# Kernel tuning notes

Hardware: AMD Instinct MI355X
Metric: run time of the kernel (lower is better)

The kernel has to match this reference:

```python
import jax, jax.numpy as jnp
import numpy as np

N_EMBD = 1024
HEAD_SIZE = 128

def setup_inputs() -> dict:
    key = jax.random.key(0)
    k1, k2, k3, k4 = jax.random.split(key, 4)
    x = jax.random.normal(k1, (8, 2048, N_EMBD), dtype=jnp.float32)
    # Linear(n_embd, head_size, bias=False): y = x @ W, W: [n_embd, head_size]
    s = 1.0 / np.sqrt(N_EMBD)
    Wk = jax.random.uniform(k2, (N_EMBD, HEAD_SIZE), jnp.float32, -s, s)
    Wq = jax.random.uniform(k3, (N_EMBD, HEAD_SIZE), jnp.float32, -s, s)
    Wv = jax.random.uniform(k4, (N_EMBD, HEAD_SIZE), jnp.float32, -s, s)
    return {"x": x, "Wk": Wk, "Wq": Wq, "Wv": Wv}

def reference(x, Wk, Wq, Wv):
    B, T, C = x.shape
    H = Wk.shape[1]
    k = jnp.einsum('btc,ch->bth', x, Wk)
    q = jnp.einsum('btc,ch->bth', x, Wq)
    v = jnp.einsum('btc,ch->bth', x, Wv)
    # scores [B, T, T], causal mask, scaled by head_size**-0.5
    wei = jnp.einsum('bqh,bkh->bqk', q, k) * (H ** -0.5)
    causal = jnp.tril(jnp.ones((T, T), dtype=bool))
    wei = jnp.where(causal, wei, -jnp.inf)
    wei = jax.nn.softmax(wei, axis=-1)
    # dropout p=0.0 (eval mode): identity
    out = jnp.einsum('bqk,bkh->bqh', wei, v)
    return out
```

## Files before the change

### kernel.cpp

```cpp
#include <hip/hip_runtime.h>
#include <hip/hip_bf16.h>
#include <stdint.h>

typedef short v8s __attribute__((ext_vector_type(8)));
typedef float v4f __attribute__((ext_vector_type(4)));
typedef float v16f __attribute__((ext_vector_type(16)));

#define N_EMBD 1024
#define HEAD 128
#define TOKENS 16384
#define T_SEQ 2048
#define BATCH 8
#define BPB 96

__device__ __forceinline__ short f2bf(float f) {
    union { float f; uint32_t u; } c; c.f = f;
    uint32_t u = c.u;
    uint32_t r = (u + 0x7fffu + ((u >> 16) & 1u)) >> 16;
    return (short)r;
}

__device__ __forceinline__ float bf2f(short s) {
    union { uint32_t u; float f; } c; c.u = ((uint32_t)(uint16_t)s) << 16;
    return c.f;
}

__global__ __launch_bounds__(256)
void wt_kernel(const float* __restrict__ Wq, const float* __restrict__ Wk,
               const float* __restrict__ Wv, short* __restrict__ wt) {
    int tid = blockIdx.x * 256 + threadIdx.x;
    int w   = tid >> 17;
    int rem = tid & 131071;
    int c = rem >> 7, h = rem & 127;
    const float* src = (w == 0) ? Wq : ((w == 1) ? Wk : Wv);
    wt[w * 131072 + h * 1024 + c] = f2bf(src[rem]);
}

__global__ __launch_bounds__(256)
void qkv_gemm(const float* __restrict__ x, const short* __restrict__ wt,
              short* __restrict__ qkv, short* __restrict__ vT) {
    const int bid = blockIdx.x;
    const int xcd = bid & 7, q = bid >> 3;
    const int mt  = xcd * 32 + q / 3;
    const int w   = q % 3;
    const int m0  = mt * 64;

    __shared__ short smem[2][64 * 40 + 128 * 40];

    const int t = threadIdx.x;
    const int lane = t & 63, wv = t >> 6;
    const int l31 = lane & 31, l1 = lane >> 5;
    const int wm = wv & 1, wn = wv >> 1;

    const short* wtw = wt + w * 131072;

    const int arow = t >> 3, ac4 = t & 7;
    const int brow = t >> 2, bc8 = t & 3;
    const float* aptr0 = x + (size_t)(m0 + arow) * 1024 + ac4 * 4;
    const float* aptr1 = x + (size_t)(m0 + arow + 32) * 1024 + ac4 * 4;
    const short* bptr0 = wtw + brow * 1024 + bc8 * 8;
    const short* bptr1 = wtw + (brow + 64) * 1024 + bc8 * 8;

    float4 af0 = *(const float4*)aptr0;
    float4 af1 = *(const float4*)aptr1;
    uint4  bf0 = *(const uint4*)bptr0;
    uint4  bf1 = *(const uint4*)bptr1;

    v16f acc[2];
    for (int i = 0; i < 16; ++i) { acc[0][i] = 0.f; acc[1][i] = 0.f; }

    {
        short* sA = smem[0]; short* sB = smem[0] + 64 * 40;
        union { short s[4]; uint64_t u; } p0, p1;
        p0.s[0] = f2bf(af0.x); p0.s[1] = f2bf(af0.y); p0.s[2] = f2bf(af0.z); p0.s[3] = f2bf(af0.w);
        p1.s[0] = f2bf(af1.x); p1.s[1] = f2bf(af1.y); p1.s[2] = f2bf(af1.z); p1.s[3] = f2bf(af1.w);
        *(uint64_t*)(&sA[arow * 40 + ac4 * 4]) = p0.u;
        *(uint64_t*)(&sA[(arow + 32) * 40 + ac4 * 4]) = p1.u;
        *(uint4*)(&sB[brow * 40 + bc8 * 8]) = bf0;
        *(uint4*)(&sB[(brow + 64) * 40 + bc8 * 8]) = bf1;
    }

    for (int it = 0; it < 32; ++it) {
        if (it < 31) {
            int kk = (it + 1) * 32;
            af0 = *(const float4*)(aptr0 + kk);
            af1 = *(const float4*)(aptr1 + kk);
            bf0 = *(const uint4*)(bptr0 + kk);
            bf1 = *(const uint4*)(bptr1 + kk);
        }
        __syncthreads();
        const short* sA = smem[it & 1];
        const short* sB = smem[it & 1] + 64 * 40;
        for (int ks = 0; ks < 2; ++ks) {
            v8s a = *(const v8s*)&sA[(wm * 32 + l31) * 40 + ks * 16 + l1 * 8];
            for (int ni = 0; ni < 2; ++ni) {
                v8s b = *(const v8s*)&sB[(wn * 64 + ni * 32 + l31) * 40 + ks * 16 + l1 * 8];
                acc[ni] = __builtin_amdgcn_mfma_f32_32x32x16_bf16(a, b, acc[ni], 0, 0, 0);
            }
        }
        if (it < 31) {
            short* nA = smem[(it + 1) & 1];
            short* nB = smem[(it + 1) & 1] + 64 * 40;
            union { short s[4]; uint64_t u; } p0, p1;
            p0.s[0] = f2bf(af0.x); p0.s[1] = f2bf(af0.y); p0.s[2] = f2bf(af0.z); p0.s[3] = f2bf(af0.w);
            p1.s[0] = f2bf(af1.x); p1.s[1] = f2bf(af1.y); p1.s[2] = f2bf(af1.z); p1.s[3] = f2bf(af1.w);
            *(uint64_t*)(&nA[arow * 40 + ac4 * 4]) = p0.u;
            *(uint64_t*)(&nA[(arow + 32) * 40 + ac4 * 4]) = p1.u;
            *(uint4*)(&nB[brow * 40 + bc8 * 8]) = bf0;
            *(uint4*)(&nB[(brow + 64) * 40 + bc8 * 8]) = bf1;
        }
    }

    if (w < 2) {
        short* outw = qkv + (size_t)w * TOKENS * HEAD;
        for (int ni = 0; ni < 2; ++ni) {
            int col = wn * 64 + ni * 32 + l31;
            for (int reg = 0; reg < 16; ++reg) {
                int m = (reg & 3) + 8 * (reg >> 2) + 4 * l1;
                outw[(size_t)(m0 + wm * 32 + m) * HEAD + col] = f2bf(acc[ni][reg]);
            }
        }
    } else {
        __syncthreads();
        short* sT = (short*)smem;
        for (int ni = 0; ni < 2; ++ni) {
            int col = wn * 64 + ni * 32 + l31;
            for (int g = 0; g < 4; ++g) {
                union { short s[4]; uint64_t u; } pk;
                for (int r = 0; r < 4; ++r) pk.s[r] = f2bf(acc[ni][g * 4 + r]);
                *(uint64_t*)(&sT[col * 72 + wm * 32 + 8 * g + 4 * l1]) = pk.u;
            }
        }
        __syncthreads();
        for (int it = 0; it < 4; ++it) {
            int c = it * 256 + t;
            int col = c >> 3, c8 = c & 7;
            uint4 d = *(const uint4*)(&sT[col * 72 + c8 * 8]);
            *(uint4*)(&vT[(size_t)col * TOKENS + m0 + c8 * 8]) = d;
        }
    }
}

__global__ __launch_bounds__(256)
void attn_kernel(const short* __restrict__ qb, const short* __restrict__ kb,
                 const short* __restrict__ vT, short* __restrict__ po,
                 float* __restrict__ pl) {
    const int bid = blockIdx.x;
    const int b  = bid & 7;
    const int r0 = bid >> 3;
    int qt2 = 0, c0 = 0;
    for (;;) { int sz = (2 * qt2 + 4) / 3; if (r0 < c0 + sz) break; c0 += sz; ++qt2; }
    const int s = r0 - c0;
    const int q0 = qt2 * 128;
    const int nkt = 2 * qt2 + 2;
    const int kt0 = s * 3;
    const int kt1 = (kt0 + 3 < nkt) ? (kt0 + 3) : nkt;

    __shared__ short sK[64 * 128];
    __shared__ short sV[128 * 64];
    __shared__ short sP[128 * 72];

    const int t = threadIdx.x;
    const int wv = t >> 6, lane = t & 63, ln = lane & 15, qd = lane >> 4;
    const int wrow0 = q0 + wv * 32;

    v8s qf[2][4];
    for (int qg = 0; qg < 2; ++qg) {
        const short* qrow = qb + ((size_t)(b * T_SEQ + wrow0 + qg * 16 + ln)) * HEAD;
        for (int ks = 0; ks < 4; ++ks)
            qf[qg][ks] = *(const v8s*)(qrow + ks * 32 + qd * 8);
    }

    v4f o[2][8] = {};
    float rs[2] = {0.f, 0.f};
    const float sc = 1.4426950408889634f / 11.313708498984761f;

    for (int kt = kt0; kt < kt1; ++kt) {
        __syncthreads();
        const short* kbase = kb + ((size_t)(b * T_SEQ + kt * 64)) * HEAD;
        for (int it = 0; it < 4; ++it) {
            int c = it * 256 + t;
            int row = c >> 4, ch = c & 15;
            uint4 d = *(const uint4*)(kbase + row * HEAD + ch * 8);
            int sch = (ch & 8) | ((ch ^ row) & 7);
            *(uint4*)(&sK[row * 128 + sch * 8]) = d;
        }
        const short* vbase = vT + (size_t)(b * T_SEQ + kt * 64);
        for (int it = 0; it < 4; ++it) {
            int c = it * 256 + t;
            int dd = c >> 3, ch = c & 7;
            uint4 d = *(const uint4*)(vbase + (size_t)dd * TOKENS + ch * 8);
            *(uint4*)(&sV[dd * 64 + ((ch ^ dd) & 7) * 8]) = d;
        }
        __syncthreads();

        if (kt * 64 >= wrow0 + 32) continue;

        v4f st[2][4] = {};
        for (int ni = 0; ni < 4; ++ni) {
            int krow = ni * 16 + ln;
            for (int ks = 0; ks < 4; ++ks) {
                int ch = ks * 4 + qd;
                v8s kf = *(const v8s*)&sK[krow * 128 + ((ch & 8) | ((ch ^ krow) & 7)) * 8];
                st[0][ni] = __builtin_amdgcn_mfma_f32_16x16x32_bf16(kf, qf[0][ks], st[0][ni], 0, 0, 0);
                st[1][ni] = __builtin_amdgcn_mfma_f32_16x16x32_bf16(kf, qf[1][ks], st[1][ni], 0, 0, 0);
            }
        }

        const bool needMask = (kt * 64 + 63 > wrow0);
        for (int qg = 0; qg < 2; ++qg) {
            int prow = wv * 32 + qg * 16 + ln;
            int qrow_g = wrow0 + qg * 16 + ln;
            for (int ni = 0; ni < 4; ++ni) {
                union { short s[4]; uint64_t u; } pk;
                for (int r = 0; r < 4; ++r) {
                    float p = exp2f(st[qg][ni][r] * sc);
                    int kg = kt * 64 + ni * 16 + qd * 4 + r;
                    if (needMask && kg > qrow_g) p = 0.f;
                    rs[qg] += p;
                    pk.s[r] = f2bf(p);
                }
                *(uint64_t*)(&sP[prow * 72 + ni * 16 + qd * 4]) = pk.u;
            }
        }

        for (int kk2 = 0; kk2 < 2; ++kk2) {
            v8s pf0 = *(const v8s*)&sP[(wv * 32 + ln) * 72 + kk2 * 32 + qd * 8];
            v8s pf1 = *(const v8s*)&sP[(wv * 32 + 16 + ln) * 72 + kk2 * 32 + qd * 8];
            for (int oni = 0; oni < 8; ++oni) {
                int dd = oni * 16 + ln;
                int ch = kk2 * 4 + qd;
                v8s vf = *(const v8s*)&sV[dd * 64 + ((ch ^ dd) & 7) * 8];
                o[0][oni] = __builtin_amdgcn_mfma_f32_16x16x32_bf16(vf, pf0, o[0][oni], 0, 0, 0);
                o[1][oni] = __builtin_amdgcn_mfma_f32_16x16x32_bf16(vf, pf1, o[1][oni], 0, 0, 0);
            }
        }
    }

    float lsum[2];
    for (int qg = 0; qg < 2; ++qg) {
        float v = rs[qg];
        v += __shfl_xor(v, 16);
        v += __shfl_xor(v, 32);
        lsum[qg] = v;
    }

    short* pob = po + (size_t)bid * 128 * 128;
    for (int qg = 0; qg < 2; ++qg)
        for (int oni = 0; oni < 8; ++oni) {
            union { short s[4]; uint2 u; } pk;
            for (int r = 0; r < 4; ++r) pk.s[r] = f2bf(o[qg][oni][r]);
            *(uint2*)(&pob[(((qg * 8 + oni) * 4 + wv) * 64 + lane) * 4]) = pk.u;
        }
    if (lane < 16)
        for (int qg = 0; qg < 2; ++qg)
            pl[bid * 128 + wv * 32 + qg * 16 + lane] = lsum[qg];
}

__global__ __launch_bounds__(256)
void combine_kernel(const short* __restrict__ po, const float* __restrict__ pl,
                    float* __restrict__ out) {
    const int bid = blockIdx.x;
    const int dh  = bid & 1;
    const int qh  = (bid >> 1) & 1;
    const int qt2 = (bid >> 2) & 15;
    const int b   = bid >> 6;
    int cum = 0;
    for (int j = 0; j < qt2; ++j) cum += (2 * j + 4) / 3;
    const int S = (2 * qt2 + 4) / 3;

    const int t = threadIdx.x;
    const int wv = t >> 6, lane = t & 63, ln = lane & 15, qd = lane >> 4;

    float l = 0.f;
    float accv[4][4] = {};

    for (int si = 0; si < S; ++si) {
        int slot = (cum + si) * 8 + b;
        l += pl[slot * 128 + wv * 32 + qh * 16 + ln];
        const short* pob = po + (size_t)slot * 16384;
        for (int oi = 0; oi < 4; ++oi) {
            int oni = dh * 4 + oi;
            union { short s[4]; uint2 u; } pk;
            pk.u = *(const uint2*)(&pob[(((qh * 8 + oni) * 4 + wv) * 64 + lane) * 4]);
            for (int r = 0; r < 4; ++r) accv[oi][r] += bf2f(pk.s[r]);
        }
    }
    float inv = 1.f / l;
    float* ob = out + ((size_t)(b * T_SEQ) + qt2 * 128 + wv * 32 + qh * 16 + ln) * HEAD;
    for (int oi = 0; oi < 4; ++oi) {
        float4 o4 = make_float4(accv[oi][0] * inv, accv[oi][1] * inv,
                                accv[oi][2] * inv, accv[oi][3] * inv);
        *(float4*)(ob + (dh * 4 + oi) * 16 + qd * 4) = o4;
    }
}

extern "C" void kernel_launch(void* const* d_in, const int* in_sizes, int n_in,
                              void* d_out, int out_size, void* d_ws, size_t ws_size,
                              hipStream_t stream) {
    const float* x  = (const float*)d_in[0];
    const float* Wk = (const float*)d_in[1];
    const float* Wq = (const float*)d_in[2];
    const float* Wv = (const float*)d_in[3];
    float* out = (float*)d_out;

    char* ws = (char*)d_ws;
    short* wt = (short*)ws;
    short* qb = (short*)(ws + 0x100000u);
    short* kb = (short*)(ws + 0x500000u);
    short* vT = (short*)(ws + 0x900000u);
    short* po = (short*)(ws + 0xD00000u);
    float* pl = (float*)(ws + 0x2500000u);
    short* qkv = qb;

    wt_kernel<<<1536, 256, 0, stream>>>(Wq, Wk, Wv, wt);
    qkv_gemm<<<768, 256, 0, stream>>>(x, wt, qkv, vT);
    attn_kernel<<<BATCH * BPB, 256, 0, stream>>>(qb, kb, vT, po, pl);
    combine_kernel<<<512, 256, 0, stream>>>(po, pl, out);
}
```

Before: 168.8 us.

## Enlarge QKV GEMM tiles and prefetch K/V tiles into registers in attention

The QKV projection GEMM moves from 64x128 tiles with a K-step of 32 to 128x128 tiles with a K-step of 64. Each wave now computes a 2x2 grid of 32x32 MFMA accumulators and the grid shrinks to 384 blocks, which improves operand reuse and halves the number of barriers. The attention kernel now loads the next K/V tile into registers after the barrier so the global loads overlap the current tile's compute, instead of loading and then storing directly. In exchange, register use rises (launch_bounds 256,2), the GEMM needs more shared memory, and fewer blocks run in the GEMM.

```diff
diff --git a/kernel.cpp b/kernel.cpp
--- a/kernel.cpp
+++ b/kernel.cpp
@@ -36,106 +36,110 @@
     wt[w * 131072 + h * 1024 + c] = f2bf(src[rem]);
 }
 
-__global__ __launch_bounds__(256)
+__global__ __launch_bounds__(256, 2)
 void qkv_gemm(const float* __restrict__ x, const short* __restrict__ wt,
               short* __restrict__ qkv, short* __restrict__ vT) {
     const int bid = blockIdx.x;
     const int xcd = bid & 7, q = bid >> 3;
-    const int mt  = xcd * 32 + q / 3;
-    const int w   = q % 3;
-    const int m0  = mt * 64;
-
-    __shared__ short smem[2][64 * 40 + 128 * 40];
+    const int mtl = q / 3, w = q % 3;
+    const int mt  = xcd * 16 + mtl;
+    const int m0  = mt * 128;
+
+    __shared__ short smem[2][256 * 72];
 
     const int t = threadIdx.x;
-    const int lane = t & 63, wv = t >> 6;
+    const int wv = t >> 6, lane = t & 63;
     const int l31 = lane & 31, l1 = lane >> 5;
     const int wm = wv & 1, wn = wv >> 1;
 
     const short* wtw = wt + w * 131072;
 
-    const int arow = t >> 3, ac4 = t & 7;
-    const int brow = t >> 2, bc8 = t & 3;
-    const float* aptr0 = x + (size_t)(m0 + arow) * 1024 + ac4 * 4;
-    const float* aptr1 = x + (size_t)(m0 + arow + 32) * 1024 + ac4 * 4;
-    const short* bptr0 = wtw + brow * 1024 + bc8 * 8;
-    const short* bptr1 = wtw + (brow + 64) * 1024 + bc8 * 8;
-
-    float4 af0 = *(const float4*)aptr0;
-    float4 af1 = *(const float4*)aptr1;
-    uint4  bf0 = *(const uint4*)bptr0;
-    uint4  bf1 = *(const uint4*)bptr1;
-
-    v16f acc[2];
-    for (int i = 0; i < 16; ++i) { acc[0][i] = 0.f; acc[1][i] = 0.f; }
+    const int ar = t >> 4, ac = t & 15;
+    const int br = t >> 3, bc = t & 7;
+    const float* aptr = x + (size_t)(m0 + ar) * 1024 + ac * 4;
+    const short* bptr = wtw + br * 1024 + bc * 8;
+
+    float4 af[8]; uint4 bfr[4];
+    for (int i = 0; i < 8; ++i) af[i] = *(const float4*)(aptr + (size_t)i * 16 * 1024);
+    for (int i = 0; i < 4; ++i) bfr[i] = *(const uint4*)(bptr + (size_t)i * 32 * 1024);
+
+    v16f acc[2][2];
+    for (int i = 0; i < 16; ++i) {
+        acc[0][0][i] = 0.f; acc[0][1][i] = 0.f; acc[1][0][i] = 0.f; acc[1][1][i] = 0.f;
+    }
 
     {
-        short* sA = smem[0]; short* sB = smem[0] + 64 * 40;
-        union { short s[4]; uint64_t u; } p0, p1;
-        p0.s[0] = f2bf(af0.x); p0.s[1] = f2bf(af0.y); p0.s[2] = f2bf(af0.z); p0.s[3] = f2bf(af0.w);
-        p1.s[0] = f2bf(af1.x); p1.s[1] = f2bf(af1.y); p1.s[2] = f2bf(af1.z); p1.s[3] = f2bf(af1.w);
-        *(uint64_t*)(&sA[arow * 40 + ac4 * 4]) = p0.u;
-        *(uint64_t*)(&sA[(arow + 32) * 40 + ac4 * 4]) = p1.u;
-        *(uint4*)(&sB[brow * 40 + bc8 * 8]) = bf0;
-        *(uint4*)(&sB[(brow + 64) * 40 + bc8 * 8]) = bf1;
-    }
-
-    for (int it = 0; it < 32; ++it) {
-        if (it < 31) {
-            int kk = (it + 1) * 32;
-            af0 = *(const float4*)(aptr0 + kk);
-            af1 = *(const float4*)(aptr1 + kk);
-            bf0 = *(const uint4*)(bptr0 + kk);
-            bf1 = *(const uint4*)(bptr1 + kk);
+        short* sA = smem[0]; short* sB = smem[0] + 128 * 72;
+        for (int i = 0; i < 8; ++i) {
+            union { short s[4]; uint64_t u; } p;
+            p.s[0] = f2bf(af[i].x); p.s[1] = f2bf(af[i].y);
+            p.s[2] = f2bf(af[i].z); p.s[3] = f2bf(af[i].w);
+            *(uint64_t*)&sA[(i * 16 + ar) * 72 + ac * 4] = p.u;
+        }
+        for (int i = 0; i < 4; ++i)
+            *(uint4*)&sB[(i * 32 + br) * 72 + bc * 8] = bfr[i];
+    }
+
+    for (int it = 0; it < 16; ++it) {
+        if (it < 15) {
+            int kk = (it + 1) * 64;
+            for (int i = 0; i < 8; ++i) af[i] = *(const float4*)(aptr + (size_t)i * 16 * 1024 + kk);
+            for (int i = 0; i < 4; ++i) bfr[i] = *(const uint4*)(bptr + (size_t)i * 32 * 1024 + kk);
         }
         __syncthreads();
         const short* sA = smem[it & 1];
-        const short* sB = smem[it & 1] + 64 * 40;
-        for (int ks = 0; ks < 2; ++ks) {
-            v8s a = *(const v8s*)&sA[(wm * 32 + l31) * 40 + ks * 16 + l1 * 8];
-            for (int ni = 0; ni < 2; ++ni) {
-                v8s b = *(const v8s*)&sB[(wn * 64 + ni * 32 + l31) * 40 + ks * 16 + l1 * 8];
-                acc[ni] = __builtin_amdgcn_mfma_f32_32x32x16_bf16(a, b, acc[ni], 0, 0, 0);
-            }
-        }
-        if (it < 31) {
+        const short* sB = smem[it & 1] + 128 * 72;
+        for (int ks = 0; ks < 4; ++ks) {
+            v8s a0 = *(const v8s*)&sA[(wm * 64 + l31) * 72 + ks * 16 + l1 * 8];
+            v8s a1 = *(const v8s*)&sA[(wm * 64 + 32 + l31) * 72 + ks * 16 + l1 * 8];
+            v8s b0 = *(const v8s*)&sB[(wn * 64 + l31) * 72 + ks * 16 + l1 * 8];
+            v8s b1 = *(const v8s*)&sB[(wn * 64 + 32 + l31) * 72 + ks * 16 + l1 * 8];
+            acc[0][0] = __builtin_amdgcn_mfma_f32_32x32x16_bf16(a0, b0, acc[0][0], 0, 0, 0);
+            acc[0][1] = __builtin_amdgcn_mfma_f32_32x32x16_bf16(a0, b1, acc[0][1], 0, 0, 0);
+            acc[1][0] = __builtin_amdgcn_mfma_f32_32x32x16_bf16(a1, b0, acc[1][0], 0, 0, 0);
+            acc[1][1] = __builtin_amdgcn_mfma_f32_32x32x16_bf16(a1, b1, acc[1][1], 0, 0, 0);
+        }
+        if (it < 15) {
             short* nA = smem[(it + 1) & 1];
-            short* nB = smem[(it + 1) & 1] + 64 * 40;
-            union { short s[4]; uint64_t u; } p0, p1;
-            p0.s[0] = f2bf(af0.x); p0.s[1] = f2bf(af0.y); p0.s[2] = f2bf(af0.z); p0.s[3] = f2bf(af0.w);
-            p1.s[0] = f2bf(af1.x); p1.s[1] = f2bf(af1.y); p1.s[2] = f2bf(af1.z); p1.s[3] = f2bf(af1.w);
-            *(uint64_t*)(&nA[arow * 40 + ac4 * 4]) = p0.u;
-            *(uint64_t*)(&nA[(arow + 32) * 40 + ac4 * 4]) = p1.u;
-            *(uint4*)(&nB[brow * 40 + bc8 * 8]) = bf0;
-            *(uint4*)(&nB[(brow + 64) * 40 + bc8 * 8]) = bf1;
+            short* nB = smem[(it + 1) & 1] + 128 * 72;
+            for (int i = 0; i < 8; ++i) {
+                union { short s[4]; uint64_t u; } p;
+                p.s[0] = f2bf(af[i].x); p.s[1] = f2bf(af[i].y);
+                p.s[2] = f2bf(af[i].z); p.s[3] = f2bf(af[i].w);
+                *(uint64_t*)&nA[(i * 16 + ar) * 72 + ac * 4] = p.u;
+            }
+            for (int i = 0; i < 4; ++i)
+                *(uint4*)&nB[(i * 32 + br) * 72 + bc * 8] = bfr[i];
         }
     }
 
     if (w < 2) {
         short* outw = qkv + (size_t)w * TOKENS * HEAD;
-        for (int ni = 0; ni < 2; ++ni) {
-            int col = wn * 64 + ni * 32 + l31;
-            for (int reg = 0; reg < 16; ++reg) {
-                int m = (reg & 3) + 8 * (reg >> 2) + 4 * l1;
-                outw[(size_t)(m0 + wm * 32 + m) * HEAD + col] = f2bf(acc[ni][reg]);
-            }
-        }
+        for (int mi = 0; mi < 2; ++mi)
+            for (int ni = 0; ni < 2; ++ni) {
+                int col = wn * 64 + ni * 32 + l31;
+                for (int reg = 0; reg < 16; ++reg) {
+                    int m = (reg & 3) + 8 * (reg >> 2) + 4 * l1;
+                    outw[(size_t)(m0 + wm * 64 + mi * 32 + m) * HEAD + col] = f2bf(acc[mi][ni][reg]);
+                }
+            }
     } else {
         __syncthreads();
         short* sT = (short*)smem;
-        for (int ni = 0; ni < 2; ++ni) {
-            int col = wn * 64 + ni * 32 + l31;
-            for (int g = 0; g < 4; ++g) {
-                union { short s[4]; uint64_t u; } pk;
-                for (int r = 0; r < 4; ++r) pk.s[r] = f2bf(acc[ni][g * 4 + r]);
-                *(uint64_t*)(&sT[col * 72 + wm * 32 + 8 * g + 4 * l1]) = pk.u;
-            }
-        }
-        __syncthreads();
-        for (int it = 0; it < 4; ++it) {
-            int c = it * 256 + t;
-            int col = c >> 3, c8 = c & 7;
-            uint4 d = *(const uint4*)(&sT[col * 72 + c8 * 8]);
+        for (int mi = 0; mi < 2; ++mi)
+            for (int ni = 0; ni < 2; ++ni) {
+                int col = wn * 64 + ni * 32 + l31;
+                for (int g = 0; g < 4; ++g) {
+                    union { short s[4]; uint64_t u; } pk;
+                    for (int r = 0; r < 4; ++r) pk.s[r] = f2bf(acc[mi][ni][g * 4 + r]);
+                    *(uint64_t*)&sT[col * 136 + wm * 64 + mi * 32 + 8 * g + 4 * l1] = pk.u;
+                }
+            }
+        __syncthreads();
+        for (int i = 0; i < 8; ++i) {
+            int c = i * 256 + t;
+            int col = c >> 4, c8 = c & 15;
+            uint4 d = *(const uint4*)(&sT[col * 136 + c8 * 8]);
             *(uint4*)(&vT[(size_t)col * TOKENS + m0 + c8 * 8]) = d;
         }
     }
@@ -171,28 +175,38 @@
             qf[qg][ks] = *(const v8s*)(qrow + ks * 32 + qd * 8);
     }
 
+    const short* kpb = kb + ((size_t)(b * T_SEQ + kt0 * 64 + (t >> 4))) * HEAD + (t & 15) * 8;
+    const short* vpb = vT + (size_t)(t >> 3) * TOKENS + b * T_SEQ + kt0 * 64 + (t & 7) * 8;
+    uint4 kpre[4], vpre[4];
+    for (int i = 0; i < 4; ++i) {
+        kpre[i] = *(const uint4*)(kpb + (size_t)i * 16 * HEAD);
+        vpre[i] = *(const uint4*)(vpb + (size_t)i * 32 * TOKENS);
+    }
+
     v4f o[2][8] = {};
     float rs[2] = {0.f, 0.f};
     const float sc = 1.4426950408889634f / 11.313708498984761f;
 
     for (int kt = kt0; kt < kt1; ++kt) {
         __syncthreads();
-        const short* kbase = kb + ((size_t)(b * T_SEQ + kt * 64)) * HEAD;
-        for (int it = 0; it < 4; ++it) {
-            int c = it * 256 + t;
-            int row = c >> 4, ch = c & 15;
-            uint4 d = *(const uint4*)(kbase + row * HEAD + ch * 8);
+        for (int i = 0; i < 4; ++i) {
+            int row = i * 16 + (t >> 4), ch = t & 15;
             int sch = (ch & 8) | ((ch ^ row) & 7);
-            *(uint4*)(&sK[row * 128 + sch * 8]) = d;
-        }
-        const short* vbase = vT + (size_t)(b * T_SEQ + kt * 64);
-        for (int it = 0; it < 4; ++it) {
-            int c = it * 256 + t;
-            int dd = c >> 3, ch = c & 7;
-            uint4 d = *(const uint4*)(vbase + (size_t)dd * TOKENS + ch * 8);
-            *(uint4*)(&sV[dd * 64 + ((ch ^ dd) & 7) * 8]) = d;
-        }
-        __syncthreads();
+            *(uint4*)(&sK[row * 128 + sch * 8]) = kpre[i];
+        }
+        for (int i = 0; i < 4; ++i) {
+            int dd = i * 32 + (t >> 3), ch = t & 7;
+            *(uint4*)(&sV[dd * 64 + ((ch ^ dd) & 7) * 8]) = vpre[i];
+        }
+        __syncthreads();
+
+        if (kt + 1 < kt1) {
+            int dk = (kt + 1 - kt0);
+            for (int i = 0; i < 4; ++i) {
+                kpre[i] = *(const uint4*)(kpb + (size_t)i * 16 * HEAD + (size_t)dk * 64 * HEAD);
+                vpre[i] = *(const uint4*)(vpb + (size_t)i * 32 * TOKENS + dk * 64);
+            }
+        }
 
         if (kt * 64 >= wrow0 + 32) continue;
 
@@ -314,7 +328,7 @@
     short* qkv = qb;
 
     wt_kernel<<<1536, 256, 0, stream>>>(Wq, Wk, Wv, wt);
-    qkv_gemm<<<768, 256, 0, stream>>>(x, wt, qkv, vT);
+    qkv_gemm<<<384, 256, 0, stream>>>(x, wt, qkv, vT);
     attn_kernel<<<BATCH * BPB, 256, 0, stream>>>(qb, kb, vT, po, pl);
     combine_kernel<<<512, 256, 0, stream>>>(po, pl, out);
 }
```

After: 202.4 us. 19.9% more time.

## Use direct global-to-LDS loads and prefetch K/V tiles in attention

Applied to the files above, without the earlier changes.

The QKV GEMM now loads the bf16 weight tile straight into LDS through global_load_lds with an XOR-swizzled 32-wide layout in place of a register round-trip. The attention kernel issues the next K tile's DMA right after the QK^T MFMAs and the next V tile's DMA after the PV MFMAs, so loads overlap compute within the single-buffered sK/sV. This cuts VGPR staging and exposed load latency. The cost is tighter barrier ordering and reliance on async LDS writes being visible at __syncthreads, which the code does not wait on explicitly.

```diff
diff --git a/kernel.cpp b/kernel.cpp
--- a/kernel.cpp
+++ b/kernel.cpp
@@ -23,6 +23,12 @@
 __device__ __forceinline__ float bf2f(short s) {
     union { uint32_t u; float f; } c; c.u = ((uint32_t)(uint16_t)s) << 16;
     return c.f;
+}
+
+__device__ __forceinline__ void dma16(const void* g, void* l) {
+    __builtin_amdgcn_global_load_lds(
+        (const __attribute__((address_space(1))) uint32_t*)g,
+        (__attribute__((address_space(3))) uint32_t*)l, 16, 0, 0);
 }
 
 __global__ __launch_bounds__(256)
@@ -45,70 +51,74 @@
     const int w   = q % 3;
     const int m0  = mt * 64;
 
-    __shared__ short smem[2][64 * 40 + 128 * 40];
+    __shared__ short smem[2][6656];
 
     const int t = threadIdx.x;
-    const int lane = t & 63, wv = t >> 6;
+    const int wv = t >> 6, lane = t & 63;
     const int l31 = lane & 31, l1 = lane >> 5;
     const int wm = wv & 1, wn = wv >> 1;
 
     const short* wtw = wt + w * 131072;
 
     const int arow = t >> 3, ac4 = t & 7;
-    const int brow = t >> 2, bc8 = t & 3;
     const float* aptr0 = x + (size_t)(m0 + arow) * 1024 + ac4 * 4;
     const float* aptr1 = x + (size_t)(m0 + arow + 32) * 1024 + ac4 * 4;
-    const short* bptr0 = wtw + brow * 1024 + bc8 * 8;
-    const short* bptr1 = wtw + (brow + 64) * 1024 + bc8 * 8;
-
-    float4 af0 = *(const float4*)aptr0;
-    float4 af1 = *(const float4*)aptr1;
-    uint4  bf0 = *(const uint4*)bptr0;
-    uint4  bf1 = *(const uint4*)bptr1;
+
+    const int bc0 = (wv * 2) * 64 + lane, bc1 = (wv * 2 + 1) * 64 + lane;
+    const int br0 = bc0 >> 2, bh0 = (bc0 & 3) ^ (br0 & 3);
+    const int br1 = bc1 >> 2, bh1 = (bc1 & 3) ^ (br1 & 3);
+    const short* bsrc0 = wtw + br0 * 1024 + bh0 * 8;
+    const short* bsrc1 = wtw + br1 * 1024 + bh1 * 8;
 
     v16f acc[2];
     for (int i = 0; i < 16; ++i) { acc[0][i] = 0.f; acc[1][i] = 0.f; }
 
     {
-        short* sA = smem[0]; short* sB = smem[0] + 64 * 40;
-        union { short s[4]; uint64_t u; } p0, p1;
-        p0.s[0] = f2bf(af0.x); p0.s[1] = f2bf(af0.y); p0.s[2] = f2bf(af0.z); p0.s[3] = f2bf(af0.w);
-        p1.s[0] = f2bf(af1.x); p1.s[1] = f2bf(af1.y); p1.s[2] = f2bf(af1.z); p1.s[3] = f2bf(af1.w);
-        *(uint64_t*)(&sA[arow * 40 + ac4 * 4]) = p0.u;
-        *(uint64_t*)(&sA[(arow + 32) * 40 + ac4 * 4]) = p1.u;
-        *(uint4*)(&sB[brow * 40 + bc8 * 8]) = bf0;
-        *(uint4*)(&sB[(brow + 64) * 40 + bc8 * 8]) = bf1;
-    }
-
+        short* sB = smem[0] + 2560;
+        dma16(bsrc0, &sB[(wv * 2) * 512]);
+        dma16(bsrc1, &sB[(wv * 2 + 1) * 512]);
+        float4 a0 = *(const float4*)aptr0;
+        float4 a1 = *(const float4*)aptr1;
+        short* sA = smem[0];
+        union { short s2[4]; uint64_t u; } p0, p1;
+        p0.s2[0] = f2bf(a0.x); p0.s2[1] = f2bf(a0.y); p0.s2[2] = f2bf(a0.z); p0.s2[3] = f2bf(a0.w);
+        p1.s2[0] = f2bf(a1.x); p1.s2[1] = f2bf(a1.y); p1.s2[2] = f2bf(a1.z); p1.s2[3] = f2bf(a1.w);
+        *(uint64_t*)&sA[arow * 40 + ac4 * 4] = p0.u;
+        *(uint64_t*)&sA[(arow + 32) * 40 + ac4 * 4] = p1.u;
+    }
+    __syncthreads();
+
+    float4 af0, af1;
     for (int it = 0; it < 32; ++it) {
+        const int cur = it & 1, nxt = cur ^ 1;
         if (it < 31) {
             int kk = (it + 1) * 32;
+            short* nB = smem[nxt] + 2560;
+            dma16(bsrc0 + kk, &nB[(wv * 2) * 512]);
+            dma16(bsrc1 + kk, &nB[(wv * 2 + 1) * 512]);
             af0 = *(const float4*)(aptr0 + kk);
             af1 = *(const float4*)(aptr1 + kk);
-            bf0 = *(const uint4*)(bptr0 + kk);
-            bf1 = *(const uint4*)(bptr1 + kk);
-        }
-        __syncthreads();
-        const short* sA = smem[it & 1];
-        const short* sB = smem[it & 1] + 64 * 40;
+        }
+        const short* sA = smem[cur];
+        const short* sB = smem[cur] + 2560;
         for (int ks = 0; ks < 2; ++ks) {
             v8s a = *(const v8s*)&sA[(wm * 32 + l31) * 40 + ks * 16 + l1 * 8];
             for (int ni = 0; ni < 2; ++ni) {
-                v8s b = *(const v8s*)&sB[(wn * 64 + ni * 32 + l31) * 40 + ks * 16 + l1 * 8];
+                int row = wn * 64 + ni * 32 + l31;
+                int sch = (ks * 2 + l1) ^ (row & 3);
+                v8s b = *(const v8s*)&sB[row * 32 + sch * 8];
                 acc[ni] = __builtin_amdgcn_mfma_f32_32x32x16_bf16(a, b, acc[ni], 0, 0, 0);
             }
         }
         if (it < 31) {
-            short* nA = smem[(it + 1) & 1];
-            short* nB = smem[(it + 1) & 1] + 64 * 40;
-            union { short s[4]; uint64_t u; } p0, p1;
-            p0.s[0] = f2bf(af0.x); p0.s[1] = f2bf(af0.y); p0.s[2] = f2bf(af0.z); p0.s[3] = f2bf(af0.w);
-            p1.s[0] = f2bf(af1.x); p1.s[1] = f2bf(af1.y); p1.s[2] = f2bf(af1.z); p1.s[3] = f2bf(af1.w);
-            *(uint64_t*)(&nA[arow * 40 + ac4 * 4]) = p0.u;
-            *(uint64_t*)(&nA[(arow + 32) * 40 + ac4 * 4]) = p1.u;
-            *(uint4*)(&nB[brow * 40 + bc8 * 8]) = bf0;
-            *(uint4*)(&nB[(brow + 64) * 40 + bc8 * 8]) = bf1;
-        }
+            short* nA = smem[nxt];
+            union { short s2[4]; uint64_t u; } p0, p1;
+            p0.s2[0] = f2bf(af0.x); p0.s2[1] = f2bf(af0.y); p0.s2[2] = f2bf(af0.z); p0.s2[3] = f2bf(af0.w);
+            p1.s2[0] = f2bf(af1.x); p1.s2[1] = f2bf(af1.y); p1.s2[2] = f2bf(af1.z); p1.s2[3] = f2bf(af1.w);
+            *(uint64_t*)&nA[arow * 40 + ac4 * 4] = p0.u;
+            *(uint64_t*)&nA[(arow + 32) * 40 + ac4 * 4] = p1.u;
+        }
+        __syncthreads();
     }
 
     if (w < 2) {
@@ -121,14 +131,13 @@
             }
         }
     } else {
-        __syncthreads();
         short* sT = (short*)smem;
         for (int ni = 0; ni < 2; ++ni) {
             int col = wn * 64 + ni * 32 + l31;
             for (int g = 0; g < 4; ++g) {
-                union { short s[4]; uint64_t u; } pk;
-                for (int r = 0; r < 4; ++r) pk.s[r] = f2bf(acc[ni][g * 4 + r]);
-                *(uint64_t*)(&sT[col * 72 + wm * 32 + 8 * g + 4 * l1]) = pk.u;
+                union { short s2[4]; uint64_t u; } pk;
+                for (int r = 0; r < 4; ++r) pk.s2[r] = f2bf(acc[ni][g * 4 + r]);
+                *(uint64_t*)&sT[col * 72 + wm * 32 + 8 * g + 4 * l1] = pk.u;
             }
         }
         __syncthreads();
@@ -171,69 +180,83 @@
             qf[qg][ks] = *(const v8s*)(qrow + ks * 32 + qd * 8);
     }
 
+    const short* kb0 = kb + ((size_t)(b * T_SEQ + kt0 * 64)) * HEAD;
+    const short* vb0 = vT + (size_t)(b * T_SEQ + kt0 * 64);
+    size_t ksrc[4], vsrc[4];
+    short *kdsts[4], *vdsts[4];
+    for (int i = 0; i < 4; ++i) {
+        int c = (wv * 4 + i) * 64 + lane;
+        int krow = c >> 4, ksch = c & 15;
+        int kch = (ksch & 8) | ((ksch ^ krow) & 7);
+        ksrc[i] = (size_t)krow * HEAD + kch * 8;
+        kdsts[i] = &sK[(wv * 4 + i) * 512];
+        int dd = c >> 3, vsch = c & 7;
+        int vch = (vsch ^ dd) & 7;
+        vsrc[i] = (size_t)dd * TOKENS + vch * 8;
+        vdsts[i] = &sV[(wv * 4 + i) * 512];
+    }
+
+    for (int i = 0; i < 4; ++i) dma16(kb0 + ksrc[i], kdsts[i]);
+    for (int i = 0; i < 4; ++i) dma16(vb0 + vsrc[i], vdsts[i]);
+    __syncthreads();
+
     v4f o[2][8] = {};
     float rs[2] = {0.f, 0.f};
     const float sc = 1.4426950408889634f / 11.313708498984761f;
 
     for (int kt = kt0; kt < kt1; ++kt) {
+        const bool active = (kt * 64 < wrow0 + 32);
+        v4f st[2][4] = {};
+        if (active) {
+            for (int ni = 0; ni < 4; ++ni) {
+                int krow = ni * 16 + ln;
+                for (int ks = 0; ks < 4; ++ks) {
+                    int ch = ks * 4 + qd;
+                    v8s kf = *(const v8s*)&sK[krow * 128 + ((ch & 8) | ((ch ^ krow) & 7)) * 8];
+                    st[0][ni] = __builtin_amdgcn_mfma_f32_16x16x32_bf16(kf, qf[0][ks], st[0][ni], 0, 0, 0);
+                    st[1][ni] = __builtin_amdgcn_mfma_f32_16x16x32_bf16(kf, qf[1][ks], st[1][ni], 0, 0, 0);
+                }
+            }
+        }
         __syncthreads();
-        const short* kbase = kb + ((size_t)(b * T_SEQ + kt * 64)) * HEAD;
-        for (int it = 0; it < 4; ++it) {
-            int c = it * 256 + t;
-            int row = c >> 4, ch = c & 15;
-            uint4 d = *(const uint4*)(kbase + row * HEAD + ch * 8);
-            int sch = (ch & 8) | ((ch ^ row) & 7);
-            *(uint4*)(&sK[row * 128 + sch * 8]) = d;
-        }
-        const short* vbase = vT + (size_t)(b * T_SEQ + kt * 64);
-        for (int it = 0; it < 4; ++it) {
-            int c = it * 256 + t;
-            int dd = c >> 3, ch = c & 7;
-            uint4 d = *(const uint4*)(vbase + (size_t)dd * TOKENS + ch * 8);
-            *(uint4*)(&sV[dd * 64 + ((ch ^ dd) & 7) * 8]) = d;
+        if (kt + 1 < kt1) {
+            const short* kbn = kb0 + (size_t)(kt + 1 - kt0) * 64 * HEAD;
+            for (int i = 0; i < 4; ++i) dma16(kbn + ksrc[i], kdsts[i]);
+        }
+
+        if (active) {
+            const bool needMask = (kt * 64 + 63 > wrow0);
+            for (int qg = 0; qg < 2; ++qg) {
+                int prow = wv * 32 + qg * 16 + ln;
+                int qrow_g = wrow0 + qg * 16 + ln;
+                for (int ni = 0; ni < 4; ++ni) {
+                    union { short s2[4]; uint64_t u; } pk;
+                    for (int r = 0; r < 4; ++r) {
+                        float p = exp2f(st[qg][ni][r] * sc);
+                        int kg = kt * 64 + ni * 16 + qd * 4 + r;
+                        if (needMask && kg > qrow_g) p = 0.f;
+                        rs[qg] += p;
+                        pk.s2[r] = f2bf(p);
+                    }
+                    *(uint64_t*)(&sP[prow * 72 + ni * 16 + qd * 4]) = pk.u;
+                }
+            }
+            for (int kk2 = 0; kk2 < 2; ++kk2) {
+                v8s pf0 = *(const v8s*)&sP[(wv * 32 + ln) * 72 + kk2 * 32 + qd * 8];
+                v8s pf1 = *(const v8s*)&sP[(wv * 32 + 16 + ln) * 72 + kk2 * 32 + qd * 8];
+                for (int oni = 0; oni < 8; ++oni) {
+                    int dd = oni * 16 + ln;
+                    int ch = kk2 * 4 + qd;
+                    v8s vf = *(const v8s*)&sV[dd * 64 + ((ch ^ dd) & 7) * 8];
+                    o[0][oni] = __builtin_amdgcn_mfma_f32_16x16x32_bf16(vf, pf0, o[0][oni], 0, 0, 0);
+                    o[1][oni] = __builtin_amdgcn_mfma_f32_16x16x32_bf16(vf, pf1, o[1][oni], 0, 0, 0);
+                }
+            }
         }
         __syncthreads();
-
-        if (kt * 64 >= wrow0 + 32) continue;
-
-        v4f st[2][4] = {};
-        for (int ni = 0; ni < 4; ++ni) {
-            int krow = ni * 16 + ln;
-            for (int ks = 0; ks < 4; ++ks) {
-                int ch = ks * 4 + qd;
-                v8s kf = *(const v8s*)&sK[krow * 128 + ((ch & 8) | ((ch ^ krow) & 7)) * 8];
-                st[0][ni] = __builtin_amdgcn_mfma_f32_16x16x32_bf16(kf, qf[0][ks], st[0][ni], 0, 0, 0);
-                st[1][ni] = __builtin_amdgcn_mfma_f32_16x16x32_bf16(kf, qf[1][ks], st[1][ni], 0, 0, 0);
-            }
-        }
-
-        const bool needMask = (kt * 64 + 63 > wrow0);
-        for (int qg = 0; qg < 2; ++qg) {
-            int prow = wv * 32 + qg * 16 + ln;
-            int qrow_g = wrow0 + qg * 16 + ln;
-            for (int ni = 0; ni < 4; ++ni) {
-                union { short s[4]; uint64_t u; } pk;
-                for (int r = 0; r < 4; ++r) {
-                    float p = exp2f(st[qg][ni][r] * sc);
-                    int kg = kt * 64 + ni * 16 + qd * 4 + r;
-                    if (needMask && kg > qrow_g) p = 0.f;
-                    rs[qg] += p;
-                    pk.s[r] = f2bf(p);
-                }
-                *(uint64_t*)(&sP[prow * 72 + ni * 16 + qd * 4]) = pk.u;
-            }
-        }
-
-        for (int kk2 = 0; kk2 < 2; ++kk2) {
-            v8s pf0 = *(const v8s*)&sP[(wv * 32 + ln) * 72 + kk2 * 32 + qd * 8];
-            v8s pf1 = *(const v8s*)&sP[(wv * 32 + 16 + ln) * 72 + kk2 * 32 + qd * 8];
-            for (int oni = 0; oni < 8; ++oni) {
-                int dd = oni * 16 + ln;
-                int ch = kk2 * 4 + qd;
-                v8s vf = *(const v8s*)&sV[dd * 64 + ((ch ^ dd) & 7) * 8];
-                o[0][oni] = __builtin_amdgcn_mfma_f32_16x16x32_bf16(vf, pf0, o[0][oni], 0, 0, 0);
-                o[1][oni] = __builtin_amdgcn_mfma_f32_16x16x32_bf16(vf, pf1, o[1][oni], 0, 0, 0);
-            }
+        if (kt + 1 < kt1) {
+            const short* vbn = vb0 + (kt + 1 - kt0) * 64;
+            for (int i = 0; i < 4; ++i) dma16(vbn + vsrc[i], vdsts[i]);
         }
     }
 
@@ -248,8 +271,8 @@
     short* pob = po + (size_t)bid * 128 * 128;
     for (int qg = 0; qg < 2; ++qg)
         for (int oni = 0; oni < 8; ++oni) {
-            union { short s[4]; uint2 u; } pk;
-            for (int r = 0; r < 4; ++r) pk.s[r] = f2bf(o[qg][oni][r]);
+            union { short s2[4]; uint2 u; } pk;
+            for (int r = 0; r < 4; ++r) pk.s2[r] = f2bf(o[qg][oni][r]);
             *(uint2*)(&pob[(((qg * 8 + oni) * 4 + wv) * 64 + lane) * 4]) = pk.u;
         }
     if (lane < 16)
@@ -281,9 +304,9 @@
         const short* pob = po + (size_t)slot * 16384;
         for (int oi = 0; oi < 4; ++oi) {
             int oni = dh * 4 + oi;
-            union { short s[4]; uint2 u; } pk;
+            union { short s2[4]; uint2 u; } pk;
             pk.u = *(const uint2*)(&pob[(((qh * 8 + oni) * 4 + wv) * 64 + lane) * 4]);
-            for (int r = 0; r < 4; ++r) accv[oi][r] += bf2f(pk.s[r]);
+            for (int r = 0; r < 4; ++r) accv[oi][r] += bf2f(pk.s2[r]);
         }
     }
     float inv = 1.f / l;
```

Result: no change. 171.7 us (+1.7%).
